# Performance work log

Hardware: AMD Instinct MI355X
Metric: run time of the kernel (lower is better)

Reference implementation:

```python
import jax, jax.numpy as jnp
import numpy as np

B, T, N, K, C = 4, 12, 2000, 8, 32
AGG_N = 4  # mean, max, min, std
EPS = 1e-5


def sparsify(a, k):
    # keep top-k entries per row, zero the rest (torch.topk + torch.where)
    thr = jax.lax.top_k(a, k)[0][..., -1:]
    return jnp.where(a < thr, jnp.zeros_like(a), a)


def aggregate(I, adj):
    # I: (b,t,n,f), adj: (b,n,n) row-sparsified with K nonzeros per row
    deg = jnp.sum(adj, axis=-1)[:, None, :, None]              # (b,1,n,1)
    mean = jnp.einsum('bnm,btmf->btnf', adj, I) / deg
    meansq = jnp.einsum('bnm,btmf->btnf', adj, I * I) / deg
    std = jnp.sqrt(jax.nn.relu(meansq - mean * mean) + EPS)
    vals, idx = jax.lax.top_k(adj, K)                          # (b,n,K)
    nb = jax.vmap(lambda Ib, ib: Ib[:, ib])(I, idx)            # (b,t,n,K,f)
    valid = (vals > 0)[:, None, :, :, None]
    mx = jnp.max(jnp.where(valid, nb, -jnp.inf), axis=3)
    mn = jnp.min(jnp.where(valid, nb, jnp.inf), axis=3)
    return jnp.concatenate([mean, mx, mn, std], axis=3)


def stower(x, adj, Theta, bias, masking, use_scalers):
    # x: (b,c,t,n) -> out: (b,o,t,n)
    I = jnp.transpose(x, (0, 2, 3, 1))                          # (b,t,n,c)
    m = aggregate(I, adj)
    if masking:
        m = jnp.where(jnp.isnan(m), 6.0, m)
        m = jnp.where(jnp.isinf(m), 0.0, m)
        m = jnp.minimum(m, 6.0)
    if use_scalers:
        deg = jnp.sum((adj > 0).astype(m.dtype), axis=-1)       # (b,n)
        s = jnp.log1p(deg)[:, None, :, None]
        m = jnp.concatenate([m, m * s, m / s], axis=3)
    out = jnp.einsum('btji,io->btjo', m, Theta) + bias
    return jnp.transpose(out, (0, 3, 1, 2))


def tcn(x, W, b):
    # tcn_layer2 with act='linear': tanh(conv1x1(x) + x)
    return jnp.tanh(jnp.einsum('oc,bctn->botn', W, x) + b[None, :, None, None] + x)


def setup_inputs():
    key = jax.random.key(0)
    ks = jax.random.split(key, 14)
    stdv = 1.0 / np.sqrt(C)
    u = lambda k, shape: jax.random.uniform(k, shape, jnp.float32, -stdv, stdv)
    return {
        'X': jax.random.normal(ks[0], (B, T, N, 1), jnp.float32),
        'adj': jax.random.uniform(ks[1], (N, N), jnp.float32),
        'adj_mask': jax.random.uniform(ks[2], (N, N), jnp.float32),
        'Theta0': u(ks[3], (AGG_N * 1, C)),   # len(agg)*len(['identity'])*in_variables
        'bias0': u(ks[4], (C,)),
        'Wt0': u(ks[5], (C, C)),
        'bt0': u(ks[6], (C,)),
        'Theta1': u(ks[7], (AGG_N * 3 * C, C)),  # len(agg)*len(scalers)*channels
        'bias1': u(ks[8], (C,)),
        'Wt1': u(ks[9], (C, C)),
        'bt1': u(ks[10], (C,)),
        'Wout': u(ks[11], (1, C)),
        'bout': u(ks[12], (1,)),
        'batch_seen': 0,
        'epoch': 0,
        'train': 0,
    }


def reference(X, adj, adj_mask, Theta0, bias0, Wt0, bt0, Theta1, bias1, Wt1, bt1, Wout, bout, batch_seen, epoch, train):
    x0 = X[:, None, :, :, 0]                                   # (b,1,t,n)
    adj_s = sparsify(jnp.broadcast_to(adj, (B, N, N)), K)
    adjm_s = sparsify(jnp.broadcast_to(adj_mask, (B, N, N)), K)
    h = stower(x0, adjm_s, Theta0, bias0, True, False)         # s_layer0 (masking, identity scaler)
    h = tcn(h, Wt0, bt0)                                       # t_layer0
    h = jax.nn.relu(stower(h, adj_s, Theta1, bias1, False, True))
    h = jax.nn.relu(tcn(h, Wt1, bt1))
    y = jnp.einsum('oc,bctn->botn', Wout, h) + bout[None, :, None, None]
    return y.reshape(B, T, N)
```

## Files before the change

kernel.cpp:

```cpp
#include <hip/hip_runtime.h>
#include <hip/hip_bf16.h>
#include <math.h>

#define BB 4
#define TT 12
#define NN 2000
#define KK 8
#define CC 32
#define EPSF 1e-5f
#define LISTCAP 16
#define NSITES (BB * TT * NN)

typedef unsigned short u16;
typedef __bf16 bf16x8 __attribute__((ext_vector_type(8)));
typedef float  f32x4  __attribute__((ext_vector_type(4)));

__device__ __forceinline__ u16 f2bf(float x) {
    union { __hip_bfloat16 h; u16 u; } c;
    c.h = __float2bfloat16(x);
    return c.u;
}
__device__ __forceinline__ float bf2f(u16 u) {
    return __uint_as_float(((unsigned)u) << 16);
}
__device__ __forceinline__ float mask6(float v) {
    if (isnan(v)) v = 6.0f;
    if (isinf(v)) v = 0.0f;
    return fminf(v, 6.0f);
}
__device__ __forceinline__ unsigned long long shflx64(unsigned long long v, int m) {
    int lo = __shfl_xor((int)(unsigned)(v & 0xffffffffull), m, 64);
    int hi = __shfl_xor((int)(unsigned)(v >> 32), m, 64);
    return ((unsigned long long)(unsigned)hi << 32) | (unsigned)lo;
}

__global__ __launch_bounds__(256)
void topk_prep(const float* __restrict__ adj, const float* __restrict__ adjm,
               int* __restrict__ t_idx, float* __restrict__ t_val,
               int* __restrict__ t_cnt, float* __restrict__ t_deg,
               float* __restrict__ t_ideg, float2* __restrict__ t_sc)
{
    __shared__ int wext[4][8];
    __shared__ int wextn[4];
    const int tid = threadIdx.x;
    const int wid = tid >> 6, lane = tid & 63;
    if (lane == 0) wextn[wid] = 0;

    const int grow = blockIdx.x * 4 + wid;
    const int mat = (grow >= NN) ? 1 : 0;
    const int row = grow - mat * NN;
    const float* src = (mat == 0 ? adjm : adj) + (size_t)row * NN;
    const float4* src4 = (const float4*)src;

    float4 v4[8];
    #pragma unroll
    for (int j = 0; j < 8; ++j) {
        const int idx4 = j * 64 + lane;
        v4[j] = (idx4 < 500) ? src4[idx4] : make_float4(0.f, 0.f, 0.f, 0.f);
    }

    unsigned long long key[8];
    #pragma unroll
    for (int j = 0; j < 8; ++j) key[j] = 0ull;

    #pragma unroll
    for (int j = 0; j < 8; ++j) {
        const float vv[4] = {v4[j].x, v4[j].y, v4[j].z, v4[j].w};
        #pragma unroll
        for (int c = 0; c < 4; ++c) {
            const unsigned e = (unsigned)((j * 64 + lane) * 4 + c);
            const unsigned long long nk =
                ((unsigned long long)__float_as_uint(vv[c]) << 32) | (unsigned)(~e);
            #pragma unroll
            for (int s = 7; s >= 1; --s)
                key[s] = (nk > key[s - 1]) ? key[s - 1] : ((nk > key[s]) ? nk : key[s]);
            if (nk > key[0]) key[0] = nk;
        }
    }

    #pragma unroll
    for (int d = 1; d < 64; d <<= 1) {
        unsigned long long ok[8], c[8];
        #pragma unroll
        for (int j = 0; j < 8; ++j) ok[j] = shflx64(key[j], d);
        #pragma unroll
        for (int j = 0; j < 8; ++j) {
            unsigned long long o = ok[7 - j];
            c[j] = (key[j] > o) ? key[j] : o;
        }
        #pragma unroll
        for (int st = 4; st >= 1; st >>= 1) {
            #pragma unroll
            for (int j = 0; j < 8; ++j) {
                if ((j & st) == 0 && (j | st) < 8) {
                    unsigned long long a = c[j], b = c[j | st];
                    unsigned long long hi = (a > b) ? a : b;
                    unsigned long long lo = (a > b) ? b : a;
                    c[j] = hi; c[j | st] = lo;
                }
            }
        }
        #pragma unroll
        for (int j = 0; j < 8; ++j) key[j] = c[j];
    }

    const float thr = __uint_as_float((unsigned)(key[7] >> 32));

    float degp = 0.f; int cp = 0;
    #pragma unroll
    for (int j = 0; j < 8; ++j) {
        const float vv[4] = {v4[j].x, v4[j].y, v4[j].z, v4[j].w};
        #pragma unroll
        for (int c = 0; c < 4; ++c) {
            const float v = vv[c];
            const bool ge = (v >= thr);
            degp += ge ? v : 0.f;
            cp   += (ge && v > 0.f) ? 1 : 0;
            if (v == thr) {
                const unsigned e = (unsigned)((j * 64 + lane) * 4 + c);
                const unsigned long long nk =
                    ((unsigned long long)__float_as_uint(v) << 32) | (unsigned)(~e);
                if (nk < key[7]) {
                    int p = atomicAdd(&wextn[wid], 1);
                    if (p < 8) wext[wid][p] = (int)e;
                }
            }
        }
    }
    #pragma unroll
    for (int off = 32; off >= 1; off >>= 1) {
        degp += __shfl_xor(degp, off, 64);
        cp   += __shfl_xor(cp, off, 64);
    }
    __syncthreads();

    if (lane == 0) {
        int en = wextn[wid]; if (en > 8) en = 8;
        const size_t ob = (size_t)grow * LISTCAP;
        #pragma unroll
        for (int j = 0; j < 8; ++j) {
            t_idx[ob + j] = (int)(~(unsigned)(key[j] & 0xffffffffull));
            t_val[ob + j] = __uint_as_float((unsigned)(key[j] >> 32));
        }
        for (int j = 0; j < 8; ++j) {
            t_idx[ob + 8 + j] = (j < en) ? wext[wid][j] : 0;
            t_val[ob + 8 + j] = (j < en) ? thr : 0.f;
        }
        t_cnt[grow]  = 8 + en;
        t_deg[grow]  = degp;
        t_ideg[grow] = 1.0f / degp;
        float s1 = log1pf((float)cp);
        t_sc[grow]   = make_float2(s1, 1.0f / s1);
    }
}

__global__ __launch_bounds__(256)
void stower0_tcn0(const float* __restrict__ X,
                  const int* __restrict__ t_idx, const float* __restrict__ t_val,
                  const int* __restrict__ t_cnt, const float* __restrict__ t_deg,
                  const float* __restrict__ Theta0, const float* __restrict__ bias0,
                  const float* __restrict__ Wt0, const float* __restrict__ bt0,
                  const float* __restrict__ Theta1, const float* __restrict__ Wt1,
                  u16* __restrict__ thHi, u16* __restrict__ thLo,
                  u16* __restrict__ wtHi, u16* __restrict__ wtLo,
                  float* __restrict__ I1)
{
    const int tid = threadIdx.x;
    if (blockIdx.x >= NSITES / 256) {
        const int pb = blockIdx.x - NSITES / 256;
        if (pb < 12) {
            const int base = pb * 1024;
            #pragma unroll
            for (int t = 0; t < 4; ++t) {
                const int i = base + t * 256 + tid;
                const int r = i >> 5, o = i & 31;
                const int jm = r >> 7, k = r & 127;
                const int tile = jm * 2 + (o >> 4), n = o & 15;
                const float v = Theta1[i];
                const u16 hi = f2bf(v);
                const int idx = (tile * 16 + n) * 128 + (((k >> 3) ^ n) << 3) + (k & 7);
                thHi[idx] = hi;
                thLo[idx] = f2bf(v - bf2f(hi));
            }
        } else {
            #pragma unroll
            for (int t = 0; t < 4; ++t) {
                const int i = t * 256 + tid;
                const float v = Wt1[i];
                const u16 hi = f2bf(v);
                wtHi[i] = hi;
                wtLo[i] = f2bf(v - bf2f(hi));
            }
        }
        return;
    }

    const int site = blockIdx.x * 256 + tid;
    const int n  = site % NN;
    const int bt = site / NN;
    const float* xrow = X + (size_t)bt * NN;

    const size_t base = (size_t)n * LISTCAP;
    const int cnt   = t_cnt[n];
    const float deg = t_deg[n];
    float wsum = 0.f, wsq = 0.f, mx = -INFINITY, mn = INFINITY;
    for (int j = 0; j < cnt; ++j) {
        int   id = t_idx[base + j];
        float w  = t_val[base + j];
        float xv = xrow[id];
        wsum = fmaf(w, xv, wsum);
        wsq  = fmaf(w * xv, xv, wsq);
        if (j < KK && w > 0.f) { mx = fmaxf(mx, xv); mn = fminf(mn, xv); }
    }
    float mean = wsum / deg;
    float var  = wsq / deg - mean * mean;
    float sd   = sqrtf(fmaxf(var, 0.f) + EPSF);
    float m0 = mask6(mean), m1 = mask6(mx), m2 = mask6(mn), m3 = mask6(sd);

    float h0[CC];
    #pragma unroll
    for (int c = 0; c < CC; ++c) {
        float v = bias0[c];
        v = fmaf(m0, Theta0[0 * CC + c], v);
        v = fmaf(m1, Theta0[1 * CC + c], v);
        v = fmaf(m2, Theta0[2 * CC + c], v);
        v = fmaf(m3, Theta0[3 * CC + c], v);
        h0[c] = v;
    }
    float* op = I1 + (size_t)site * CC;
    #pragma unroll
    for (int c = 0; c < CC; ++c) {
        float acc = bt0[c] + h0[c];
        #pragma unroll
        for (int k = 0; k < CC; ++k) acc = fmaf(Wt0[c * CC + k], h0[k], acc);
        op[c] = tanhf(acc);
    }
}

__global__ __launch_bounds__(256)
void stower1_agg(const float* __restrict__ I1,
                 const int* __restrict__ t_idx, const float* __restrict__ t_val,
                 const int* __restrict__ t_cnt, const float* __restrict__ t_ideg,
                 u16* __restrict__ mHi, u16* __restrict__ mLo)
{
    const int tid  = threadIdx.x;
    const int site = blockIdx.x * 8 + (tid >> 5);
    const int f    = tid & 31;
    const int n  = site % NN;
    const int bt = site / NN;
    const size_t rbase = (size_t)(NN + n) * LISTCAP;
    const int cnt    = t_cnt[NN + n];
    const float ideg = t_ideg[NN + n];
    const float* Ibt = I1 + (size_t)bt * NN * CC;

    const int4   i0 = *(const int4*)&t_idx[rbase];
    const int4   i1 = *(const int4*)&t_idx[rbase + 4];
    const float4 w0 = *(const float4*)&t_val[rbase];
    const float4 w1 = *(const float4*)&t_val[rbase + 4];

    const float x0 = Ibt[(size_t)i0.x * CC + f];
    const float x1 = Ibt[(size_t)i0.y * CC + f];
    const float x2 = Ibt[(size_t)i0.z * CC + f];
    const float x3 = Ibt[(size_t)i0.w * CC + f];
    const float x4 = Ibt[(size_t)i1.x * CC + f];
    const float x5 = Ibt[(size_t)i1.y * CC + f];
    const float x6 = Ibt[(size_t)i1.z * CC + f];
    const float x7 = Ibt[(size_t)i1.w * CC + f];

    float wsum = 0.f, wsq = 0.f, mx = -INFINITY, mn = INFINITY;
    #define AGG(wv, xv) do { \
        wsum = fmaf(wv, xv, wsum); wsq = fmaf(wv * xv, xv, wsq); \
        mx = fmaxf(mx, xv); mn = fminf(mn, xv); } while (0)
    AGG(w0.x, x0); AGG(w0.y, x1); AGG(w0.z, x2); AGG(w0.w, x3);
    AGG(w1.x, x4); AGG(w1.y, x5); AGG(w1.z, x6); AGG(w1.w, x7);
    #undef AGG
    if (cnt > 8) {
        for (int j = 8; j < cnt; ++j) {
            int   id = t_idx[rbase + j];
            float wv = t_val[rbase + j];
            float xv = Ibt[(size_t)id * CC + f];
            wsum = fmaf(wv, xv, wsum);
            wsq  = fmaf(wv * xv, xv, wsq);
        }
    }
    const float mean = wsum * ideg;
    const float var  = wsq * ideg - mean * mean;
    const float sd   = sqrtf(fmaxf(var, 0.f) + EPSF);

    const int sx = site & 15;
    const int b  = site * 128;
    const int fh = f >> 3, fl = f & 7;
    const int ia  = b + (((0  + fh) ^ sx) << 3) + fl;
    const int ib  = b + (((4  + fh) ^ sx) << 3) + fl;
    const int ic  = b + (((8  + fh) ^ sx) << 3) + fl;
    const int id_ = b + (((12 + fh) ^ sx) << 3) + fl;
    u16 h0 = f2bf(mean); mHi[ia]  = h0; mLo[ia]  = f2bf(mean - bf2f(h0));
    u16 h1 = f2bf(mx);   mHi[ib]  = h1; mLo[ib]  = f2bf(mx   - bf2f(h1));
    u16 h2 = f2bf(mn);   mHi[ic]  = h2; mLo[ic]  = f2bf(mn   - bf2f(h2));
    u16 h3 = f2bf(sd);   mHi[id_] = h3; mLo[id_] = f2bf(sd   - bf2f(h3));
}

__global__ __launch_bounds__(256, 3)
void stower1_gemm(const u16* __restrict__ mHi, const u16* __restrict__ mLo,
                  const u16* __restrict__ thHi, const u16* __restrict__ thLo,
                  const u16* __restrict__ wtHi, const u16* __restrict__ wtLo,
                  const float2* __restrict__ t_sc,
                  const float* __restrict__ bias1, const float* __restrict__ bt1,
                  const float* __restrict__ Wout, const float* __restrict__ bout,
                  float* __restrict__ out)
{
    __shared__ u16 sBlo[96 * 128];
    __shared__ alignas(16) u16 uSpace[12288];
    __shared__ float sPart[64];

    u16*   mT  = uSpace;
    u16*   hHi = uSpace;
    u16*   hLo = hHi + 32 * 40;
    float* h32 = (float*)((char*)uSpace + 5120);

    const int tid  = threadIdx.x;
    const int lane = tid & 63;
    const int w    = tid >> 6;
    const int m15  = lane & 15;
    const int q    = lane >> 4;
    const int hf   = w & 1;
    const int st   = w >> 1;
    const int ot   = w >> 1;
    const int st2  = w & 1;

    for (int i = tid; i < 1536; i += 256)
        ((float4*)uSpace)[i] = ((const float4*)thHi)[i];
    __syncthreads();
    bf16x8 bH[3][4];
    #pragma unroll
    for (int j3 = 0; j3 < 3; ++j3) {
        const int tile = 2 * j3 + hf;
        #pragma unroll
        for (int ks = 0; ks < 4; ++ks)
            bH[j3][ks] = *(const bf16x8*)&uSpace[(tile * 16 + m15) * 128 +
                                                 (((ks * 4 + q) ^ m15) << 3)];
    }
    __syncthreads();
    for (int i = tid; i < 1536; i += 256)
        ((float4*)sBlo)[i] = ((const float4*)thLo)[i];
    const bf16x8 bwh = *(const bf16x8*)&wtHi[(ot * 16 + m15) * 32 + q * 8];
    const bf16x8 bwl = *(const bf16x8*)&wtLo[(ot * 16 + m15) * 32 + q * 8];
    const float b1o   = bias1[hf * 16 + m15];
    const float bt1o  = bt1[ot * 16 + m15];
    const float wouto = Wout[ot * 16 + m15];
    const float boutv = bout[0];

    #pragma unroll 1
    for (int mb = 0; mb < 3; ++mb) {
        const int sbase = (blockIdx.x * 3 + mb) * 32;

        {
            const float4* gh = (const float4*)&mHi[(size_t)sbase * 128];
            const float4* gl = (const float4*)&mLo[(size_t)sbase * 128];
            float4* dh = (float4*)mT;
            float4* dl = (float4*)(mT + 4096);
            dh[tid]       = gh[tid];
            dh[tid + 256] = gh[tid + 256];
            dl[tid]       = gl[tid];
            dl[tid + 256] = gl[tid + 256];
        }
        __syncthreads();

        f32x4 acc[3];
        #pragma unroll
        for (int j3 = 0; j3 < 3; ++j3) acc[j3] = (f32x4){0.f, 0.f, 0.f, 0.f};
        const int arow = (st * 16 + m15) * 128;
        #pragma unroll
        for (int ks = 0; ks < 4; ++ks) {
            const int koff = (((ks * 4 + q) ^ m15) << 3);
            const bf16x8 aH = *(const bf16x8*)&mT[arow + koff];
            const bf16x8 aL = *(const bf16x8*)&mT[4096 + arow + koff];
            #pragma unroll
            for (int j3 = 0; j3 < 3; ++j3) {
                const bf16x8 bL = *(const bf16x8*)&sBlo[((2 * j3 + hf) * 16 + m15) * 128 + koff];
                acc[j3] = __builtin_amdgcn_mfma_f32_16x16x32_bf16(aH, bH[j3][ks], acc[j3], 0, 0, 0);
                acc[j3] = __builtin_amdgcn_mfma_f32_16x16x32_bf16(aH, bL,          acc[j3], 0, 0, 0);
                acc[j3] = __builtin_amdgcn_mfma_f32_16x16x32_bf16(aL, bH[j3][ks], acc[j3], 0, 0, 0);
            }
        }
        __syncthreads();

        #pragma unroll
        for (int r = 0; r < 4; ++r) {
            const int sl2  = st * 16 + q * 4 + r;
            const int site = sbase + sl2;
            const int n    = site % NN;
            const float2 sc = t_sc[NN + n];
            float h = acc[0][r] + sc.x * acc[1][r] + sc.y * acc[2][r] + b1o;
            h = fmaxf(h, 0.f);
            const int o = hf * 16 + m15;
            const u16 hi = f2bf(h);
            hHi[sl2 * 40 + o] = hi;
            hLo[sl2 * 40 + o] = f2bf(h - bf2f(hi));
            h32[sl2 * 33 + o] = h;
        }
        __syncthreads();

        f32x4 c2 = (f32x4){0.f, 0.f, 0.f, 0.f};
        {
            const bf16x8 ahh = *(const bf16x8*)&hHi[(st2 * 16 + m15) * 40 + q * 8];
            const bf16x8 ahl = *(const bf16x8*)&hLo[(st2 * 16 + m15) * 40 + q * 8];
            c2 = __builtin_amdgcn_mfma_f32_16x16x32_bf16(ahh, bwh, c2, 0, 0, 0);
            c2 = __builtin_amdgcn_mfma_f32_16x16x32_bf16(ahh, bwl, c2, 0, 0, 0);
            c2 = __builtin_amdgcn_mfma_f32_16x16x32_bf16(ahl, bwh, c2, 0, 0, 0);
        }
        float p[4];
        #pragma unroll
        for (int r = 0; r < 4; ++r) {
            const int sl2 = st2 * 16 + q * 4 + r;
            const float hres = h32[sl2 * 33 + ot * 16 + m15];
            float yv = tanhf(c2[r] + bt1o + hres);
            yv = fmaxf(yv, 0.f);
            p[r] = yv * wouto;
            #pragma unroll
            for (int mk = 1; mk <= 8; mk <<= 1)
                p[r] += __shfl_xor(p[r], mk, 64);
        }
        float selv  = (m15 & 1) ? p[1] : p[0];
        float selv2 = (m15 & 1) ? p[3] : p[2];
        selv = (m15 & 2) ? selv2 : selv;
        if (m15 < 4) sPart[ot * 32 + st2 * 16 + q * 4 + m15] = selv;
        __syncthreads();

        if (tid < 32) out[sbase + tid] = sPart[tid] + sPart[32 + tid] + boutv;
    }
}

extern "C" void kernel_launch(void* const* d_in, const int* in_sizes, int n_in,
                              void* d_out, int out_size, void* d_ws, size_t ws_size,
                              hipStream_t stream)
{
    const float* X      = (const float*)d_in[0];
    const float* adj    = (const float*)d_in[1];
    const float* adjm   = (const float*)d_in[2];
    const float* Theta0 = (const float*)d_in[3];
    const float* bias0  = (const float*)d_in[4];
    const float* Wt0    = (const float*)d_in[5];
    const float* bt0    = (const float*)d_in[6];
    const float* Theta1 = (const float*)d_in[7];
    const float* bias1  = (const float*)d_in[8];
    const float* Wt1    = (const float*)d_in[9];
    const float* bt1    = (const float*)d_in[10];
    const float* Wout   = (const float*)d_in[11];
    const float* bout   = (const float*)d_in[12];
    (void)in_sizes; (void)n_in; (void)out_size; (void)ws_size;

    char* p = (char*)d_ws;
    int*    t_idx  = (int*)p;    p += (size_t)2 * NN * LISTCAP * sizeof(int);
    float*  t_val  = (float*)p;  p += (size_t)2 * NN * LISTCAP * sizeof(float);
    int*    t_cnt  = (int*)p;    p += (size_t)2 * NN * sizeof(int);
    float*  t_deg  = (float*)p;  p += (size_t)2 * NN * sizeof(float);
    float*  t_ideg = (float*)p;  p += (size_t)2 * NN * sizeof(float);
    float2* t_sc   = (float2*)p; p += (size_t)2 * NN * sizeof(float2);
    float*  I1     = (float*)p;  p += (size_t)NSITES * CC * sizeof(float);
    u16*    mHi    = (u16*)p;    p += (size_t)NSITES * 128 * sizeof(u16);
    u16*    mLo    = (u16*)p;    p += (size_t)NSITES * 128 * sizeof(u16);
    u16*    thHi   = (u16*)p;    p += (size_t)96 * 128 * sizeof(u16);
    u16*    thLo   = (u16*)p;    p += (size_t)96 * 128 * sizeof(u16);
    u16*    wtHi   = (u16*)p;    p += (size_t)1024 * sizeof(u16);
    u16*    wtLo   = (u16*)p;    p += (size_t)1024 * sizeof(u16);

    hipLaunchKernelGGL(topk_prep, dim3(2 * NN / 4), dim3(256), 0, stream,
                       adj, adjm, t_idx, t_val, t_cnt, t_deg, t_ideg, t_sc);
    hipLaunchKernelGGL(stower0_tcn0, dim3(NSITES / 256 + 13), dim3(256), 0, stream,
                       X, t_idx, t_val, t_cnt, t_deg, Theta0, bias0, Wt0, bt0,
                       Theta1, Wt1, thHi, thLo, wtHi, wtLo, I1);
    hipLaunchKernelGGL(stower1_agg, dim3(NSITES / 8), dim3(256), 0, stream,
                       I1, t_idx, t_val, t_cnt, t_ideg, mHi, mLo);
    hipLaunchKernelGGL(stower1_gemm, dim3(NSITES / 96), dim3(256), 0, stream,
                       mHi, mLo, thHi, thLo, wtHi, wtLo, t_sc,
                       bias1, bt1, Wout, bout, (float*)d_out);
}
```

Measured before the change: 184.3 us.

## Use one block per row in top-k prep with float sorting networks

```diff
diff --git a/kernel.cpp b/kernel.cpp
--- a/kernel.cpp
+++ b/kernel.cpp
@@ -28,11 +28,6 @@
     if (isinf(v)) v = 0.0f;
     return fminf(v, 6.0f);
 }
-__device__ __forceinline__ unsigned long long shflx64(unsigned long long v, int m) {
-    int lo = __shfl_xor((int)(unsigned)(v & 0xffffffffull), m, 64);
-    int hi = __shfl_xor((int)(unsigned)(v >> 32), m, 64);
-    return ((unsigned long long)(unsigned)hi << 32) | (unsigned)lo;
-}
 
 __global__ __launch_bounds__(256)
 void topk_prep(const float* __restrict__ adj, const float* __restrict__ adjm,
@@ -40,62 +35,61 @@
                int* __restrict__ t_cnt, float* __restrict__ t_deg,
                float* __restrict__ t_ideg, float2* __restrict__ t_sc)
 {
-    __shared__ int wext[4][8];
-    __shared__ int wextn[4];
-    const int tid = threadIdx.x;
-    const int wid = tid >> 6, lane = tid & 63;
-    if (lane == 0) wextn[wid] = 0;
-
-    const int grow = blockIdx.x * 4 + wid;
+    __shared__ float sTop[4][8];
+    __shared__ float sDeg[4];
+    __shared__ int   sCp[4];
+    __shared__ int   sStrictIdx[8];
+    __shared__ float sStrictVal[8];
+    __shared__ int   sTieIdx[16];
+    __shared__ int   nStrict, nTie;
+    __shared__ float sThr;
+
+    const int tid  = threadIdx.x;
+    const int lane = tid & 63;
+    const int wid  = tid >> 6;
+
+    const int grow = blockIdx.x;
     const int mat = (grow >= NN) ? 1 : 0;
     const int row = grow - mat * NN;
     const float* src = (mat == 0 ? adjm : adj) + (size_t)row * NN;
     const float4* src4 = (const float4*)src;
 
-    float4 v4[8];
-    #pragma unroll
-    for (int j = 0; j < 8; ++j) {
-        const int idx4 = j * 64 + lane;
-        v4[j] = (idx4 < 500) ? src4[idx4] : make_float4(0.f, 0.f, 0.f, 0.f);
-    }
-
-    unsigned long long key[8];
-    #pragma unroll
-    for (int j = 0; j < 8; ++j) key[j] = 0ull;
-
-    #pragma unroll
-    for (int j = 0; j < 8; ++j) {
-        const float vv[4] = {v4[j].x, v4[j].y, v4[j].z, v4[j].w};
-        #pragma unroll
-        for (int c = 0; c < 4; ++c) {
-            const unsigned e = (unsigned)((j * 64 + lane) * 4 + c);
-            const unsigned long long nk =
-                ((unsigned long long)__float_as_uint(vv[c]) << 32) | (unsigned)(~e);
-            #pragma unroll
-            for (int s = 7; s >= 1; --s)
-                key[s] = (nk > key[s - 1]) ? key[s - 1] : ((nk > key[s]) ? nk : key[s]);
-            if (nk > key[0]) key[0] = nk;
-        }
-    }
-
+    if (tid == 0) { nStrict = 0; nTie = 0; }
+
+    const float4 v0 = src4[tid];
+    const float4 v1 = (tid < 244) ? src4[256 + tid]
+                                  : make_float4(-1.f, -1.f, -1.f, -1.f);
+    const float vv[8] = {v0.x, v0.y, v0.z, v0.w, v1.x, v1.y, v1.z, v1.w};
+
+    float a[8];
+    #pragma unroll
+    for (int j = 0; j < 8; ++j) a[j] = vv[j];
+    #define CE(i, j) { float _mx = fmaxf(a[i], a[j]); float _mn = fminf(a[i], a[j]); a[i] = _mx; a[j] = _mn; }
+    CE(0,1) CE(2,3) CE(4,5) CE(6,7)
+    CE(0,2) CE(1,3) CE(4,6) CE(5,7)
+    CE(1,2) CE(5,6)
+    CE(0,4) CE(1,5) CE(2,6) CE(3,7)
+    CE(2,4) CE(3,5)
+    CE(1,2) CE(3,4) CE(5,6)
+    #undef CE
+
+    float key[8];
+    #pragma unroll
+    for (int j = 0; j < 8; ++j) key[j] = a[j];
     #pragma unroll
     for (int d = 1; d < 64; d <<= 1) {
-        unsigned long long ok[8], c[8];
-        #pragma unroll
-        for (int j = 0; j < 8; ++j) ok[j] = shflx64(key[j], d);
-        #pragma unroll
-        for (int j = 0; j < 8; ++j) {
-            unsigned long long o = ok[7 - j];
-            c[j] = (key[j] > o) ? key[j] : o;
-        }
+        float ok[8], c[8];
+        #pragma unroll
+        for (int j = 0; j < 8; ++j) ok[j] = __shfl_xor(key[j], d, 64);
+        #pragma unroll
+        for (int j = 0; j < 8; ++j) c[j] = fmaxf(key[j], ok[7 - j]);
         #pragma unroll
         for (int st = 4; st >= 1; st >>= 1) {
             #pragma unroll
             for (int j = 0; j < 8; ++j) {
                 if ((j & st) == 0 && (j | st) < 8) {
-                    unsigned long long a = c[j], b = c[j | st];
-                    unsigned long long hi = (a > b) ? a : b;
-                    unsigned long long lo = (a > b) ? b : a;
+                    float hi = fmaxf(c[j], c[j | st]);
+                    float lo = fminf(c[j], c[j | st]);
                     c[j] = hi; c[j | st] = lo;
                 }
             }
@@ -103,28 +97,47 @@
         #pragma unroll
         for (int j = 0; j < 8; ++j) key[j] = c[j];
     }
-
-    const float thr = __uint_as_float((unsigned)(key[7] >> 32));
+    if (lane == 0) {
+        #pragma unroll
+        for (int j = 0; j < 8; ++j) sTop[wid][j] = key[j];
+    }
+    __syncthreads();
+
+    if (tid == 0) {
+        int p0 = 0, p1 = 0, p2 = 0, p3 = 0;
+        float t = -1.f;
+        for (int r = 0; r < 8; ++r) {
+            const float c0 = (p0 < 8) ? sTop[0][p0] : -2.f;
+            const float c1 = (p1 < 8) ? sTop[1][p1] : -2.f;
+            const float c2 = (p2 < 8) ? sTop[2][p2] : -2.f;
+            const float c3 = (p3 < 8) ? sTop[3][p3] : -2.f;
+            float bv = c0; int best = 0;
+            if (c1 > bv) { bv = c1; best = 1; }
+            if (c2 > bv) { bv = c2; best = 2; }
+            if (c3 > bv) { bv = c3; best = 3; }
+            if (best == 0) ++p0; else if (best == 1) ++p1;
+            else if (best == 2) ++p2; else ++p3;
+            t = bv;
+        }
+        sThr = t;
+    }
+    __syncthreads();
+    const float thr = sThr;
 
     float degp = 0.f; int cp = 0;
     #pragma unroll
-    for (int j = 0; j < 8; ++j) {
-        const float vv[4] = {v4[j].x, v4[j].y, v4[j].z, v4[j].w};
-        #pragma unroll
-        for (int c = 0; c < 4; ++c) {
-            const float v = vv[c];
-            const bool ge = (v >= thr);
-            degp += ge ? v : 0.f;
-            cp   += (ge && v > 0.f) ? 1 : 0;
-            if (v == thr) {
-                const unsigned e = (unsigned)((j * 64 + lane) * 4 + c);
-                const unsigned long long nk =
-                    ((unsigned long long)__float_as_uint(v) << 32) | (unsigned)(~e);
-                if (nk < key[7]) {
-                    int p = atomicAdd(&wextn[wid], 1);
-                    if (p < 8) wext[wid][p] = (int)e;
-                }
-            }
+    for (int s = 0; s < 8; ++s) {
+        const float v = vv[s];
+        const int e = (s < 4) ? (tid * 4 + s) : ((256 + tid) * 4 + (s - 4));
+        const bool ge = (v >= thr);
+        degp += ge ? v : 0.f;
+        cp   += (ge && v > 0.f) ? 1 : 0;
+        if (v > thr) {
+            int p = atomicAdd(&nStrict, 1);
+            if (p < 8) { sStrictIdx[p] = e; sStrictVal[p] = v; }
+        } else if (v == thr) {
+            int p = atomicAdd(&nTie, 1);
+            if (p < 16) sTieIdx[p] = e;
         }
     }
     #pragma unroll
@@ -132,24 +145,39 @@
         degp += __shfl_xor(degp, off, 64);
         cp   += __shfl_xor(cp, off, 64);
     }
+    if (lane == 0) { sDeg[wid] = degp; sCp[wid] = cp; }
     __syncthreads();
 
-    if (lane == 0) {
-        int en = wextn[wid]; if (en > 8) en = 8;
+    if (tid == 0) {
+        const float deg = sDeg[0] + sDeg[1] + sDeg[2] + sDeg[3];
+        const int cnt_pos = sCp[0] + sCp[1] + sCp[2] + sCp[3];
+        int m = nStrict; if (m > 8) m = 8;
+        int nt = nTie;   if (nt > 16) nt = 16;
+        for (int i = 1; i < nt; ++i) {
+            int v = sTieIdx[i]; int j = i - 1;
+            while (j >= 0 && sTieIdx[j] > v) { sTieIdx[j + 1] = sTieIdx[j]; --j; }
+            sTieIdx[j + 1] = v;
+        }
         const size_t ob = (size_t)grow * LISTCAP;
-        #pragma unroll
-        for (int j = 0; j < 8; ++j) {
-            t_idx[ob + j] = (int)(~(unsigned)(key[j] & 0xffffffffull));
-            t_val[ob + j] = __uint_as_float((unsigned)(key[j] >> 32));
-        }
-        for (int j = 0; j < 8; ++j) {
-            t_idx[ob + 8 + j] = (j < en) ? wext[wid][j] : 0;
-            t_val[ob + 8 + j] = (j < en) ? thr : 0.f;
-        }
-        t_cnt[grow]  = 8 + en;
-        t_deg[grow]  = degp;
-        t_ideg[grow] = 1.0f / degp;
-        float s1 = log1pf((float)cp);
+        for (int j = 0; j < m; ++j) {
+            t_idx[ob + j] = sStrictIdx[j];
+            t_val[ob + j] = sStrictVal[j];
+        }
+        const int need = 8 - m;
+        for (int j = 0; j < need; ++j) {
+            t_idx[ob + m + j] = sTieIdx[j];
+            t_val[ob + m + j] = thr;
+        }
+        int extra = nt - need;
+        if (extra > 8) extra = 8; if (extra < 0) extra = 0;
+        for (int j = 0; j < extra; ++j) {
+            t_idx[ob + 8 + j] = sTieIdx[need + j];
+            t_val[ob + 8 + j] = thr;
+        }
+        t_cnt[grow]  = 8 + extra;
+        t_deg[grow]  = deg;
+        t_ideg[grow] = 1.0f / deg;
+        const float s1 = log1pf((float)cnt_pos);
         t_sc[grow]   = make_float2(s1, 1.0f / s1);
     }
 }
@@ -465,7 +493,7 @@
     u16*    wtHi   = (u16*)p;    p += (size_t)1024 * sizeof(u16);
     u16*    wtLo   = (u16*)p;    p += (size_t)1024 * sizeof(u16);
 
-    hipLaunchKernelGGL(topk_prep, dim3(2 * NN / 4), dim3(256), 0, stream,
+    hipLaunchKernelGGL(topk_prep, dim3(2 * NN), dim3(256), 0, stream,
                        adj, adjm, t_idx, t_val, t_cnt, t_deg, t_ideg, t_sc);
     hipLaunchKernelGGL(stower0_tcn0, dim3(NSITES / 256 + 13), dim3(256), 0, stream,
                        X, t_idx, t_val, t_cnt, t_deg, Theta0, bias0, Wt0, bt0,
```

Result: faster. 177.1 us (-3.9%).
